# Kernel optimization log

Hardware: AMD Instinct MI355X
Metric: run time of the kernel (lower is better)

## Reference

```python
import jax, jax.numpy as jnp
import numpy as np

DIM = 64      # fixed by fuse=BasicConv2d(64,64)
HEADS = 8
B, H, W = 16, 128, 128
CPH = DIM // HEADS  # 8 channels per head


def conv2d(x, w, groups=1, pad=1):
    # x: [B,C,H,W], w: [O, C//groups, kh, kw]
    return jax.lax.conv_general_dilated(
        x, w, window_strides=(1, 1), padding=[(pad, pad), (pad, pad)],
        dimension_numbers=("NCHW", "OIHW", "NCHW"), feature_group_count=groups)


def setup_inputs() -> dict:
    key = jax.random.key(0)
    ks = jax.random.split(key, 8)
    y = jax.random.normal(ks[0], (B, DIM, H, W), jnp.float32)
    # conv3d kernels collapse to their middle depth slice (depth-1 input, zero pad)
    w_qkv = jax.random.normal(ks[1], (3 * DIM, DIM), jnp.float32) * 0.05        # 1x1x1 qkv
    w_dw = jax.random.normal(ks[2], (3 * DIM, 1, 3, 3), jnp.float32) * 0.1      # depthwise 3x3
    w_proj = jax.random.normal(ks[3], (DIM, DIM), jnp.float32) * 0.05           # 1x1x1 project_out
    w_fc = jax.random.normal(ks[4], (9, 3 * HEADS), jnp.float32) * 0.1          # fc: 24->9
    b_fc = jnp.zeros((9,), jnp.float32)
    w_dep = jax.random.normal(ks[5], (DIM, 9, 3, 3), jnp.float32) * 0.1         # grouped: 72->64, groups=8
    b_dep = jnp.zeros((DIM,), jnp.float32)
    temperature = jnp.ones((HEADS, 1, 1), jnp.float32)
    w_fuse = jax.random.normal(ks[6], (DIM, DIM, 3, 3), jnp.float32) * 0.05     # fuse conv, no bias
    bn_gamma = jnp.ones((DIM,), jnp.float32)
    bn_beta = jnp.zeros((DIM,), jnp.float32)
    bn_mean = jnp.zeros((DIM,), jnp.float32)
    bn_var = jnp.ones((DIM,), jnp.float32)
    return dict(y=y, w_qkv=w_qkv, w_dw=w_dw, w_proj=w_proj, w_fc=w_fc, b_fc=b_fc,
                w_dep=w_dep, b_dep=b_dep, temperature=temperature, w_fuse=w_fuse,
                bn_gamma=bn_gamma, bn_beta=bn_beta, bn_mean=bn_mean, bn_var=bn_var)


def reference(y, w_qkv, w_dw, w_proj, w_fc, b_fc, w_dep, b_dep, temperature,
              w_fuse, bn_gamma, bn_beta, bn_mean, bn_var):
    b, c, h, w = y.shape
    # qkv 1x1 conv then 3x3 depthwise conv (groups = 3*DIM)
    qkv = jnp.einsum('oc,bchw->bohw', w_qkv, y)                 # [b,192,h,w]
    qkv = conv2d(qkv, w_dw, groups=3 * DIM, pad=1)
    # dynamic kernel generation branch: flat reshape (row-major, matches torch)
    f_all = qkv.reshape(b, h * w, 3 * HEADS, CPH).transpose(0, 2, 1, 3)  # [b,24,hw,8]
    f_all = jnp.einsum('oc,bcne->bone', w_fc, f_all) + b_fc[None, :, None, None]  # [b,9,hw,8]
    f_conv = f_all.transpose(0, 3, 1, 2).reshape(b, 9 * CPH, h, w)       # [b,72,h,w]
    out_conv = conv2d(f_conv, w_dep, groups=CPH, pad=1) + b_dep[None, :, None, None]
    # channel (transposed) attention with L2-normalize + temperature + softmax
    q, k, v = jnp.split(qkv, 3, axis=1)
    def to_heads(t):
        return t.reshape(b, HEADS, CPH, h * w)
    q, k, v = to_heads(q), to_heads(k), to_heads(v)
    q = q / jnp.maximum(jnp.linalg.norm(q, axis=-1, keepdims=True), 1e-12)
    k = k / jnp.maximum(jnp.linalg.norm(k, axis=-1, keepdims=True), 1e-12)
    attn = jnp.einsum('bhcn,bhdn->bhcd', q, k) * temperature[None]       # [b,8,8,8]
    attn = jax.nn.softmax(attn, axis=-1)
    out = jnp.einsum('bhcd,bhdn->bhcn', attn, v).reshape(b, DIM, h, w)
    out = jnp.einsum('oc,bchw->bohw', w_proj, out)
    output = out + out_conv
    # fuse: conv3x3 (no bias) + BatchNorm (inference stats), then residual + ReLU
    fused = conv2d(output, w_fuse, pad=1)
    scale = (bn_gamma / jnp.sqrt(bn_var + 1e-5))[None, :, None, None]
    fused = (fused - bn_mean[None, :, None, None]) * scale + bn_beta[None, :, None, None]
    return jax.nn.relu(fused + y)
```

## Files before the change

kernel.cpp:

```cpp
#include <hip/hip_runtime.h>
#include <hip/hip_bf16.h>

#define BN 16
#define CC 64
#define HH 128
#define WW 128
#define HW 16384
#define C3 192
#define NHEADS 8


__global__ __launch_bounds__(256) void k_qkv1(const float* __restrict__ y,
                                              const float* __restrict__ w_qkv,
                                              float* __restrict__ out, int chunk) {
    __shared__ float ws[64 * 64];
    int tid = threadIdx.x;
    for (int i = tid; i < 4096; i += 256) {
        int c = i >> 6, o = i & 63;
        ws[i] = w_qkv[(chunk * 64 + o) * 64 + c];
    }
    __syncthreads();
    int bid = blockIdx.x;
    int b = bid >> 6;
    int ptile = bid & 63;
    int pxg = tid & 127;
    int osub = tid >> 7;
    int p0 = ptile * 256 + pxg * 2;
    const float* yb = y + (size_t)b * CC * HW + p0;
    float acc0[32];
    float acc1[32];
#pragma unroll
    for (int o = 0; o < 32; ++o) { acc0[o] = 0.f; acc1[o] = 0.f; }
    for (int c = 0; c < 64; ++c) {
        float2 yv = *(const float2*)(yb + (size_t)c * HW);
        const float* wr = &ws[c * 64 + osub * 32];
#pragma unroll
        for (int o = 0; o < 32; ++o) {
            float w = wr[o];
            acc0[o] = fmaf(w, yv.x, acc0[o]);
            acc1[o] = fmaf(w, yv.y, acc1[o]);
        }
    }
    float* ob = out + (size_t)b * 64 * HW + (size_t)(osub * 32) * HW + p0;
#pragma unroll
    for (int o = 0; o < 32; ++o) {
        *(float2*)(ob + (size_t)o * HW) = make_float2(acc0[o], acc1[o]);
    }
}

__global__ __launch_bounds__(256) void k_dw(const float* __restrict__ in,
                                            const float* __restrict__ w_dw,
                                            float* __restrict__ out, int chunk) {
    int bid = blockIdx.x;
    int tid = threadIdx.x;
    int b = bid >> 11;
    int rem = bid & 2047;
    int ch = rem >> 5;
    int tile = rem & 31;
    int pp = tile * 512 + tid * 2;
    int py = pp >> 7, px = pp & 127;
    const float* ib = in + ((size_t)b * 64 + ch) * HW;
    const float* wr = w_dw + (chunk * 64 + ch) * 9;
    float w[9];
#pragma unroll
    for (int i = 0; i < 9; ++i) w[i] = wr[i];
    float a0 = 0.f, a1 = 0.f;
#pragma unroll
    for (int ky = 0; ky < 3; ++ky) {
        int yy = py + ky - 1;
        bool yok = (unsigned)yy < 128u;
#pragma unroll
        for (int kx = 0; kx < 4; ++kx) {
            int xx = px + kx - 1;
            bool ok = yok && ((unsigned)xx < 128u);
            float v = ok ? ib[yy * 128 + xx] : 0.f;
            if (kx < 3) a0 = fmaf(w[ky * 3 + kx], v, a0);
            if (kx > 0) a1 = fmaf(w[ky * 3 + kx - 1], v, a1);
        }
    }
    *(float2*)(out + ((size_t)b * C3 + chunk * 64 + ch) * HW + pp) = make_float2(a0, a1);
}

__global__ __launch_bounds__(256) void k_fc(const float* __restrict__ qkv,
                                            const float* __restrict__ w_fc,
                                            const float* __restrict__ b_fc,
                                            float* __restrict__ fconv) {
    __shared__ float wf[216];
    __shared__ float bf[9];
    int tid = threadIdx.x;
    if (tid < 216) wf[tid] = w_fc[tid];
    if (tid < 9) bf[tid] = b_fc[tid];
    __syncthreads();
    int bid = blockIdx.x;
    int b = bid >> 9;
    int rem = bid & 511;
    int n = rem * 32 + (tid >> 3);
    int e = tid & 7;
    const float* x = qkv + (size_t)b * C3 * HW + (size_t)n * 192 + e;
    float xe[24];
#pragma unroll
    for (int g = 0; g < 24; ++g) xe[g] = x[g * 8];
    float* ob = fconv + (size_t)b * 72 * HW + n;
#pragma unroll
    for (int o = 0; o < 9; ++o) {
        float acc = bf[o];
#pragma unroll
        for (int g = 0; g < 24; ++g) acc = fmaf(wf[o * 24 + g], xe[g], acc);
        ob[(size_t)(e * 9 + o) * HW] = acc;
    }
}

#define GST 20
__global__ __launch_bounds__(256) void k_gconv(const float* __restrict__ fconv,
                                               const float* __restrict__ w_dep,
                                               const float* __restrict__ b_dep,
                                               float* __restrict__ outO) {
    __shared__ __align__(16) float sm_in[9 * 18 * GST];
    __shared__ __align__(16) float sm_w[81 * 8];
    __shared__ float sm_b[8];
    int tid = threadIdx.x;
    int bid = blockIdx.x;
    int b = bid >> 9;
    int rem = bid & 511;
    int grp = rem >> 6;
    int tile = rem & 63;
    int ty0 = (tile >> 3) * 16, tx0 = (tile & 7) * 16;
    const float* ibase = fconv + ((size_t)b * 72 + grp * 9) * HW;
    for (int i = tid; i < 9 * 324; i += 256) {
        int c = i / 324;
        int r2 = i - c * 324;
        int r = r2 / 18;
        int q = r2 - r * 18;
        int yy = ty0 + r - 1, xx = tx0 + q - 1;
        sm_in[c * (18 * GST) + r * GST + q] =
            ((unsigned)yy < 128u && (unsigned)xx < 128u)
                ? ibase[(size_t)c * HW + yy * 128 + xx] : 0.f;
    }
    for (int i = tid; i < 648; i += 256) {
        int o = i & 7;
        int ik = i >> 3;
        sm_w[i] = w_dep[(size_t)(grp * 8 + o) * 81 + ik];
    }
    if (tid < 8) sm_b[tid] = b_dep[grp * 8 + tid];
    __syncthreads();
    int row = tid >> 4, col = tid & 15;
    float acc[8];
#pragma unroll
    for (int o = 0; o < 8; ++o) acc[o] = sm_b[o];
#pragma unroll
    for (int ic = 0; ic < 9; ++ic) {
        float nb[3][3];
        const float* sc = &sm_in[ic * (18 * GST) + row * GST + col];
#pragma unroll
        for (int r = 0; r < 3; ++r)
#pragma unroll
            for (int q = 0; q < 3; ++q) nb[r][q] = sc[r * GST + q];
        const float* wp = &sm_w[ic * 72];
#pragma unroll
        for (int k = 0; k < 9; ++k) {
            float4 w0 = *(const float4*)(wp + k * 8);
            float4 w1 = *(const float4*)(wp + k * 8 + 4);
            float v = nb[k / 3][k % 3];
            acc[0] = fmaf(w0.x, v, acc[0]);
            acc[1] = fmaf(w0.y, v, acc[1]);
            acc[2] = fmaf(w0.z, v, acc[2]);
            acc[3] = fmaf(w0.w, v, acc[3]);
            acc[4] = fmaf(w1.x, v, acc[4]);
            acc[5] = fmaf(w1.y, v, acc[5]);
            acc[6] = fmaf(w1.z, v, acc[6]);
            acc[7] = fmaf(w1.w, v, acc[7]);
        }
    }
    float* ob = outO + ((size_t)b * 64 + grp * 8) * HW + (ty0 + row) * 128 + tx0 + col;
#pragma unroll
    for (int o = 0; o < 8; ++o) ob[(size_t)o * HW] = acc[o];
}

__global__ __launch_bounds__(256) void k_attn(const float* __restrict__ qkv,
                                              const float* __restrict__ temperature,
                                              float* __restrict__ attn) {
    __shared__ float red[4][64];
    __shared__ float redq[4][8];
    __shared__ float redk[4][8];
    __shared__ float sm_inv[16];
    __shared__ float lg[64];
    int bid = blockIdx.x;
    int b = bid >> 3, h = bid & 7;
    int tid = threadIdx.x;
    const float* Q = qkv + ((size_t)b * C3 + h * 8) * HW;
    const float* K = Q + (size_t)64 * HW;
    float acc[64], qs[8], ks[8];
#pragma unroll
    for (int j = 0; j < 64; ++j) acc[j] = 0.f;
#pragma unroll
    for (int d = 0; d < 8; ++d) { qs[d] = 0.f; ks[d] = 0.f; }
    for (int i = tid; i < HW; i += 256) {
        float qv[8], kv[8];
#pragma unroll
        for (int d = 0; d < 8; ++d) {
            qv[d] = Q[(size_t)d * HW + i];
            kv[d] = K[(size_t)d * HW + i];
        }
#pragma unroll
        for (int d = 0; d < 8; ++d) {
            qs[d] = fmaf(qv[d], qv[d], qs[d]);
            ks[d] = fmaf(kv[d], kv[d], ks[d]);
        }
#pragma unroll
        for (int c = 0; c < 8; ++c)
#pragma unroll
            for (int d = 0; d < 8; ++d)
                acc[c * 8 + d] = fmaf(qv[c], kv[d], acc[c * 8 + d]);
    }
#pragma unroll
    for (int j = 0; j < 64; ++j) {
#pragma unroll
        for (int off = 32; off; off >>= 1) acc[j] += __shfl_down(acc[j], off, 64);
    }
#pragma unroll
    for (int d = 0; d < 8; ++d) {
#pragma unroll
        for (int off = 32; off; off >>= 1) {
            qs[d] += __shfl_down(qs[d], off, 64);
            ks[d] += __shfl_down(ks[d], off, 64);
        }
    }
    int lane = tid & 63, wv = tid >> 6;
    if (lane == 0) {
#pragma unroll
        for (int j = 0; j < 64; ++j) red[wv][j] = acc[j];
#pragma unroll
        for (int d = 0; d < 8; ++d) { redq[wv][d] = qs[d]; redk[wv][d] = ks[d]; }
    }
    __syncthreads();
    if (tid < 16) {
        int d = tid & 7;
        float s = (tid < 8) ? (redq[0][d] + redq[1][d] + redq[2][d] + redq[3][d])
                            : (redk[0][d] + redk[1][d] + redk[2][d] + redk[3][d]);
        sm_inv[tid] = 1.f / fmaxf(sqrtf(s), 1e-12f);
    }
    __syncthreads();
    if (tid < 64) {
        float s = red[0][tid] + red[1][tid] + red[2][tid] + red[3][tid];
        int c = tid >> 3, d = tid & 7;
        lg[tid] = s * sm_inv[c] * sm_inv[8 + d] * temperature[h];
    }
    __syncthreads();
    if (tid < 8) {
        int c = tid;
        float m = lg[c * 8];
#pragma unroll
        for (int d = 1; d < 8; ++d) m = fmaxf(m, lg[c * 8 + d]);
        float ssum = 0.f, ex[8];
#pragma unroll
        for (int d = 0; d < 8; ++d) { ex[d] = expf(lg[c * 8 + d] - m); ssum += ex[d]; }
        float inv = 1.f / ssum;
#pragma unroll
        for (int d = 0; d < 8; ++d)
            attn[((size_t)(b * 8 + h) * 8 + c) * 8 + d] = ex[d] * inv;
    }
}

__global__ __launch_bounds__(256) void k_av_proj(const float* __restrict__ qkv,
                                                 const float* __restrict__ attn,
                                                 const float* __restrict__ w_proj,
                                                 float* __restrict__ outO) {
    __shared__ float at[512];
    __shared__ float wp[4096];
    int tid = threadIdx.x;
    int bid = blockIdx.x;
    int b = bid >> 6, tile = bid & 63;
    for (int i = tid; i < 512; i += 256) at[i] = attn[b * 512 + i];
    for (int i = tid; i < 4096; i += 256) {
        int c = i >> 6, o = i & 63;
        wp[i] = w_proj[o * 64 + c];
    }
    __syncthreads();
    int p = tile * 256 + tid;
    const float* vb = qkv + ((size_t)b * C3 + 128) * HW + p;
    float av[64];
#pragma unroll
    for (int h = 0; h < 8; ++h) {
        float vv[8];
#pragma unroll
        for (int d = 0; d < 8; ++d) vv[d] = vb[(size_t)(h * 8 + d) * HW];
#pragma unroll
        for (int ci = 0; ci < 8; ++ci) {
            float s = 0.f;
#pragma unroll
            for (int d = 0; d < 8; ++d) s = fmaf(at[(h * 8 + ci) * 8 + d], vv[d], s);
            av[h * 8 + ci] = s;
        }
    }
    float* ob = outO + (size_t)b * 64 * HW + p;
    float acc[64];
#pragma unroll
    for (int o = 0; o < 64; ++o) acc[o] = ob[(size_t)o * HW];
    for (int c = 0; c < 64; ++c) {
        float a = av[c];
        const float* wr = &wp[c * 64];
#pragma unroll
        for (int o = 0; o < 64; ++o) acc[o] = fmaf(wr[o], a, acc[o]);
    }
#pragma unroll
    for (int o = 0; o < 64; ++o) ob[(size_t)o * HW] = acc[o];
}

#define ST 20
__global__ __launch_bounds__(256) void k_fuse(const float* __restrict__ outO,
                                              const float* __restrict__ w_fuse,
                                              const float* __restrict__ bn_gamma,
                                              const float* __restrict__ bn_beta,
                                              const float* __restrict__ bn_mean,
                                              const float* __restrict__ bn_var,
                                              const float* __restrict__ y,
                                              float* __restrict__ dout) {
    __shared__ __align__(16) float sm_in[8 * 18 * ST];
    __shared__ __align__(16) float sm_w[8 * 9 * 64];
    __shared__ float sm_sc[64];
    __shared__ float sm_sb[64];
    int tid = threadIdx.x;
    int bid = blockIdx.x;
    int b = bid >> 6;
    int tile = bid & 63;
    int ty0 = (tile >> 3) * 16, tx0 = (tile & 7) * 16;

    if (tid < 64) {
        float sc = bn_gamma[tid] * rsqrtf(bn_var[tid] + 1e-5f);
        sm_sc[tid] = sc;
        sm_sb[tid] = bn_beta[tid] - bn_mean[tid] * sc;
    }

    int osub = tid >> 6;
    int o0 = osub * 16;
    int lane = tid & 63;
    int col = lane & 15;
    int rowg = lane >> 4;
    int r0 = rowg * 4;

    const float* ib = outO + (size_t)b * 64 * HW;
    float acc[4][16];
#pragma unroll
    for (int p = 0; p < 4; ++p)
#pragma unroll
        for (int o = 0; o < 16; ++o) acc[p][o] = 0.f;

    for (int ch = 0; ch < 8; ++ch) {
        int c0 = ch * 8;
        __syncthreads();
        for (int i = tid; i < 8 * 18 * 18; i += 256) {
            int c = i / 324;
            int rem = i - c * 324;
            int r = rem / 18;
            int q = rem - r * 18;
            int yy = ty0 + r - 1;
            int xx = tx0 + q - 1;
            float v = ((unsigned)yy < 128u && (unsigned)xx < 128u)
                          ? ib[(size_t)(c0 + c) * HW + yy * 128 + xx] : 0.f;
            sm_in[c * (18 * ST) + r * ST + q] = v;
        }
        for (int i = tid; i < 8 * 9 * 64; i += 256) {
            int o = i & 63;
            int kk = (i >> 6) % 9;
            int c = i / 576;
            sm_w[(c * 9 + kk) * 64 + o] = w_fuse[((size_t)o * 64 + (c0 + c)) * 9 + kk];
        }
        __syncthreads();
        for (int cc = 0; cc < 8; ++cc) {
            float nb[6][3];
            const float* sin_c = &sm_in[cc * (18 * ST)];
#pragma unroll
            for (int r = 0; r < 6; ++r)
#pragma unroll
                for (int q = 0; q < 3; ++q)
                    nb[r][q] = sin_c[(r0 + r) * ST + col + q];
            const float* wc = &sm_w[cc * 576 + o0];
#pragma unroll
            for (int k = 0; k < 9; ++k) {
                int ky = k / 3, kx = k % 3;
                float4 w0 = *(const float4*)(wc + k * 64);
                float4 w1 = *(const float4*)(wc + k * 64 + 4);
                float4 w2 = *(const float4*)(wc + k * 64 + 8);
                float4 w3 = *(const float4*)(wc + k * 64 + 12);
#pragma unroll
                for (int p = 0; p < 4; ++p) {
                    float v = nb[p + ky][kx];
                    acc[p][0]  = fmaf(w0.x, v, acc[p][0]);
                    acc[p][1]  = fmaf(w0.y, v, acc[p][1]);
                    acc[p][2]  = fmaf(w0.z, v, acc[p][2]);
                    acc[p][3]  = fmaf(w0.w, v, acc[p][3]);
                    acc[p][4]  = fmaf(w1.x, v, acc[p][4]);
                    acc[p][5]  = fmaf(w1.y, v, acc[p][5]);
                    acc[p][6]  = fmaf(w1.z, v, acc[p][6]);
                    acc[p][7]  = fmaf(w1.w, v, acc[p][7]);
                    acc[p][8]  = fmaf(w2.x, v, acc[p][8]);
                    acc[p][9]  = fmaf(w2.y, v, acc[p][9]);
                    acc[p][10] = fmaf(w2.z, v, acc[p][10]);
                    acc[p][11] = fmaf(w2.w, v, acc[p][11]);
                    acc[p][12] = fmaf(w3.x, v, acc[p][12]);
                    acc[p][13] = fmaf(w3.y, v, acc[p][13]);
                    acc[p][14] = fmaf(w3.z, v, acc[p][14]);
                    acc[p][15] = fmaf(w3.w, v, acc[p][15]);
                }
            }
        }
    }
#pragma unroll
    for (int o = 0; o < 16; ++o) {
        int og = o0 + o;
        float sc = sm_sc[og], sb = sm_sb[og];
#pragma unroll
        for (int p = 0; p < 4; ++p) {
            int pyy = ty0 + r0 + p;
            int pxx = tx0 + col;
            size_t idx = ((size_t)b * 64 + og) * HW + pyy * 128 + pxx;
            float v = acc[p][o] * sc + sb + y[idx];
            dout[idx] = fmaxf(v, 0.f);
        }
    }
}

extern "C" void kernel_launch(void* const* d_in, const int* in_sizes, int n_in,
                              void* d_out, int out_size, void* d_ws, size_t ws_size,
                              hipStream_t stream) {
    const float* y           = (const float*)d_in[0];
    const float* w_qkv       = (const float*)d_in[1];
    const float* w_dw        = (const float*)d_in[2];
    const float* w_proj      = (const float*)d_in[3];
    const float* w_fc        = (const float*)d_in[4];
    const float* b_fc        = (const float*)d_in[5];
    const float* w_dep       = (const float*)d_in[6];
    const float* b_dep       = (const float*)d_in[7];
    const float* temperature = (const float*)d_in[8];
    const float* w_fuse      = (const float*)d_in[9];
    const float* bn_gamma    = (const float*)d_in[10];
    const float* bn_beta     = (const float*)d_in[11];
    const float* bn_mean     = (const float*)d_in[12];
    const float* bn_var      = (const float*)d_in[13];
    float* out = (float*)d_out;

    float* ws    = (float*)d_ws;
    float* qkvB  = ws;
    float* bufT  = ws + 25165824;
    float* bufO  = ws + 34603008;
    float* attn  = ws + 42992640;
    (void)in_sizes; (void)n_in; (void)out_size; (void)ws_size;

    for (int g = 0; g < 2; ++g) {
        const float* yg = y + (size_t)g * 8 * CC * HW;
        float* outg = out + (size_t)g * 8 * CC * HW;
        for (int chunk = 0; chunk < 3; ++chunk) {
            k_qkv1<<<512, 256, 0, stream>>>(yg, w_qkv, bufT, chunk);
            k_dw<<<16384, 256, 0, stream>>>(bufT, w_dw, qkvB, chunk);
        }
        k_fc<<<4096, 256, 0, stream>>>(qkvB, w_fc, b_fc, bufT);
        k_gconv<<<4096, 256, 0, stream>>>(bufT, w_dep, b_dep, bufO);
        k_attn<<<64, 256, 0, stream>>>(qkvB, temperature, attn);
        k_av_proj<<<512, 256, 0, stream>>>(qkvB, attn, w_proj, bufO);
        k_fuse<<<512, 256, 0, stream>>>(bufO, w_fuse, bn_gamma, bn_beta,
                                        bn_mean, bn_var, yg, outg);
    }
}
```

Measured before the change: 1.045 ms.

## Fuse qkv 1x1 conv with depthwise 3x3 via haloed tiles; split fuse conv outputs

Replaces the separate qkv pointwise GEMM and depthwise conv launches with one kernel. Each block computes the 1x1 projection for a 16x16 tile plus its halo into shared memory, then applies the 3x3 depthwise filter there, so the intermediate never goes through global memory. The cost is recomputing the halo pixels (324 vs 256 per tile) and re-reading y once per group of 32 output channels. Separately, the fuse conv now splits its 64 output channels across two blocks, doubling the grid to raise occupancy and cut registers per thread, at the price of loading the input tile twice.

New measurement: 2.017 ms. +93.0%, slower.

```diff
diff --git a/kernel.cpp b/kernel.cpp
--- a/kernel.cpp
+++ b/kernel.cpp
@@ -10,75 +10,85 @@
 #define NHEADS 8
 
 
-__global__ __launch_bounds__(256) void k_qkv1(const float* __restrict__ y,
-                                              const float* __restrict__ w_qkv,
-                                              float* __restrict__ out, int chunk) {
-    __shared__ float ws[64 * 64];
-    int tid = threadIdx.x;
-    for (int i = tid; i < 4096; i += 256) {
-        int c = i >> 6, o = i & 63;
-        ws[i] = w_qkv[(chunk * 64 + o) * 64 + c];
-    }
-    __syncthreads();
-    int bid = blockIdx.x;
-    int b = bid >> 6;
-    int ptile = bid & 63;
-    int pxg = tid & 127;
-    int osub = tid >> 7;
-    int p0 = ptile * 256 + pxg * 2;
-    const float* yb = y + (size_t)b * CC * HW + p0;
-    float acc0[32];
-    float acc1[32];
+__global__ __launch_bounds__(256) void k_qkvdw(const float* __restrict__ y,
+                                               const float* __restrict__ w_qkv,
+                                               const float* __restrict__ w_dw,
+                                               float* __restrict__ qkvB) {
+    __shared__ __align__(16) float sm_w1[64 * 32];
+    __shared__ __align__(16) float sm_y[8 * 324];
+    __shared__ __align__(16) float sm_q[32 * 324];
+    __shared__ float sm_wd[32 * 9];
+    int tid = threadIdx.x;
+    int bid = blockIdx.x;
+    int b = bid / 384;
+    int rem = bid - b * 384;
+    int tile = rem / 6;
+    int q32 = rem - tile * 6;
+    int ty0 = (tile >> 3) * 16, tx0 = (tile & 7) * 16;
+
+    for (int i = tid; i < 2048; i += 256) {
+        int c = i >> 5, o = i & 31;
+        sm_w1[i] = w_qkv[(size_t)(q32 * 32 + o) * 64 + c];
+    }
+    for (int i = tid; i < 288; i += 256)
+        sm_wd[i] = w_dw[(size_t)(q32 * 32) * 9 + i];
+
+    const float* yb = y + (size_t)b * CC * HW;
+    float acc0[32], acc1[32];
 #pragma unroll
     for (int o = 0; o < 32; ++o) { acc0[o] = 0.f; acc1[o] = 0.f; }
-    for (int c = 0; c < 64; ++c) {
-        float2 yv = *(const float2*)(yb + (size_t)c * HW);
-        const float* wr = &ws[c * 64 + osub * 32];
-#pragma unroll
-        for (int o = 0; o < 32; ++o) {
-            float w = wr[o];
-            acc0[o] = fmaf(w, yv.x, acc0[o]);
-            acc1[o] = fmaf(w, yv.y, acc1[o]);
-        }
-    }
-    float* ob = out + (size_t)b * 64 * HW + (size_t)(osub * 32) * HW + p0;
+    bool p2 = tid < 68;
+
+    for (int c8 = 0; c8 < 8; ++c8) {
+        __syncthreads();
+        for (int i = tid; i < 2592; i += 256) {
+            int c = i / 324;
+            int p = i - c * 324;
+            int r = p / 18, q = p - r * 18;
+            int yy = ty0 + r - 1, xx = tx0 + q - 1;
+            sm_y[i] = ((unsigned)yy < 128u && (unsigned)xx < 128u)
+                          ? yb[(size_t)(c8 * 8 + c) * HW + yy * 128 + xx] : 0.f;
+        }
+        __syncthreads();
+#pragma unroll
+        for (int cc = 0; cc < 8; ++cc) {
+            float yv0 = sm_y[cc * 324 + tid];
+            float yv1 = p2 ? sm_y[cc * 324 + 256 + tid] : 0.f;
+            const float* wr = &sm_w1[(c8 * 8 + cc) * 32];
+#pragma unroll
+            for (int o4 = 0; o4 < 8; ++o4) {
+                float4 w = *(const float4*)(wr + o4 * 4);
+                acc0[o4 * 4 + 0] = fmaf(w.x, yv0, acc0[o4 * 4 + 0]);
+                acc0[o4 * 4 + 1] = fmaf(w.y, yv0, acc0[o4 * 4 + 1]);
+                acc0[o4 * 4 + 2] = fmaf(w.z, yv0, acc0[o4 * 4 + 2]);
+                acc0[o4 * 4 + 3] = fmaf(w.w, yv0, acc0[o4 * 4 + 3]);
+                acc1[o4 * 4 + 0] = fmaf(w.x, yv1, acc1[o4 * 4 + 0]);
+                acc1[o4 * 4 + 1] = fmaf(w.y, yv1, acc1[o4 * 4 + 1]);
+                acc1[o4 * 4 + 2] = fmaf(w.z, yv1, acc1[o4 * 4 + 2]);
+                acc1[o4 * 4 + 3] = fmaf(w.w, yv1, acc1[o4 * 4 + 3]);
+            }
+        }
+    }
 #pragma unroll
     for (int o = 0; o < 32; ++o) {
-        *(float2*)(ob + (size_t)o * HW) = make_float2(acc0[o], acc1[o]);
-    }
-}
-
-__global__ __launch_bounds__(256) void k_dw(const float* __restrict__ in,
-                                            const float* __restrict__ w_dw,
-                                            float* __restrict__ out, int chunk) {
-    int bid = blockIdx.x;
-    int tid = threadIdx.x;
-    int b = bid >> 11;
-    int rem = bid & 2047;
-    int ch = rem >> 5;
-    int tile = rem & 31;
-    int pp = tile * 512 + tid * 2;
-    int py = pp >> 7, px = pp & 127;
-    const float* ib = in + ((size_t)b * 64 + ch) * HW;
-    const float* wr = w_dw + (chunk * 64 + ch) * 9;
-    float w[9];
-#pragma unroll
-    for (int i = 0; i < 9; ++i) w[i] = wr[i];
-    float a0 = 0.f, a1 = 0.f;
-#pragma unroll
-    for (int ky = 0; ky < 3; ++ky) {
-        int yy = py + ky - 1;
-        bool yok = (unsigned)yy < 128u;
-#pragma unroll
-        for (int kx = 0; kx < 4; ++kx) {
-            int xx = px + kx - 1;
-            bool ok = yok && ((unsigned)xx < 128u);
-            float v = ok ? ib[yy * 128 + xx] : 0.f;
-            if (kx < 3) a0 = fmaf(w[ky * 3 + kx], v, a0);
-            if (kx > 0) a1 = fmaf(w[ky * 3 + kx - 1], v, a1);
-        }
-    }
-    *(float2*)(out + ((size_t)b * C3 + chunk * 64 + ch) * HW + pp) = make_float2(a0, a1);
+        sm_q[o * 324 + tid] = acc0[o];
+        if (p2) sm_q[o * 324 + 256 + tid] = acc1[o];
+    }
+    __syncthreads();
+    int row = tid >> 4, col = tid & 15;
+    float* ob = qkvB + ((size_t)b * C3 + q32 * 32) * HW
+                + (ty0 + row) * 128 + tx0 + col;
+    for (int ch = 0; ch < 32; ++ch) {
+        const float* sq = &sm_q[ch * 324 + row * 18 + col];
+        const float* wd = &sm_wd[ch * 9];
+        float a = 0.f;
+#pragma unroll
+        for (int dy = 0; dy < 3; ++dy)
+#pragma unroll
+            for (int dx = 0; dx < 3; ++dx)
+                a = fmaf(wd[dy * 3 + dx], sq[dy * 18 + dx], a);
+        ob[(size_t)ch * HW] = a;
+    }
 }
 
 __global__ __launch_bounds__(256) void k_fc(const float* __restrict__ qkv,
@@ -316,13 +326,15 @@
                                               const float* __restrict__ y,
                                               float* __restrict__ dout) {
     __shared__ __align__(16) float sm_in[8 * 18 * ST];
-    __shared__ __align__(16) float sm_w[8 * 9 * 64];
+    __shared__ __align__(16) float sm_w[8 * 9 * 32];
     __shared__ float sm_sc[64];
     __shared__ float sm_sb[64];
     int tid = threadIdx.x;
     int bid = blockIdx.x;
-    int b = bid >> 6;
-    int tile = bid & 63;
+    int b = bid >> 7;
+    int rem = bid & 127;
+    int ob32 = rem >> 6;
+    int tile = rem & 63;
     int ty0 = (tile >> 3) * 16, tx0 = (tile & 7) * 16;
 
     if (tid < 64) {
@@ -332,38 +344,39 @@
     }
 
     int osub = tid >> 6;
-    int o0 = osub * 16;
+    int o0 = osub * 8;
     int lane = tid & 63;
     int col = lane & 15;
     int rowg = lane >> 4;
     int r0 = rowg * 4;
 
     const float* ib = outO + (size_t)b * 64 * HW;
-    float acc[4][16];
+    float acc[4][8];
 #pragma unroll
     for (int p = 0; p < 4; ++p)
 #pragma unroll
-        for (int o = 0; o < 16; ++o) acc[p][o] = 0.f;
+        for (int o = 0; o < 8; ++o) acc[p][o] = 0.f;
 
     for (int ch = 0; ch < 8; ++ch) {
         int c0 = ch * 8;
         __syncthreads();
         for (int i = tid; i < 8 * 18 * 18; i += 256) {
             int c = i / 324;
-            int rem = i - c * 324;
-            int r = rem / 18;
-            int q = rem - r * 18;
+            int rem2 = i - c * 324;
+            int r = rem2 / 18;
+            int q = rem2 - r * 18;
             int yy = ty0 + r - 1;
             int xx = tx0 + q - 1;
             float v = ((unsigned)yy < 128u && (unsigned)xx < 128u)
                           ? ib[(size_t)(c0 + c) * HW + yy * 128 + xx] : 0.f;
             sm_in[c * (18 * ST) + r * ST + q] = v;
         }
-        for (int i = tid; i < 8 * 9 * 64; i += 256) {
-            int o = i & 63;
-            int kk = (i >> 6) % 9;
-            int c = i / 576;
-            sm_w[(c * 9 + kk) * 64 + o] = w_fuse[((size_t)o * 64 + (c0 + c)) * 9 + kk];
+        for (int i = tid; i < 8 * 9 * 32; i += 256) {
+            int o = i & 31;
+            int kk = (i >> 5) % 9;
+            int c = i / 288;
+            sm_w[(c * 9 + kk) * 32 + o] =
+                w_fuse[((size_t)(ob32 * 32 + o) * 64 + (c0 + c)) * 9 + kk];
         }
         __syncthreads();
         for (int cc = 0; cc < 8; ++cc) {
@@ -374,40 +387,30 @@
 #pragma unroll
                 for (int q = 0; q < 3; ++q)
                     nb[r][q] = sin_c[(r0 + r) * ST + col + q];
-            const float* wc = &sm_w[cc * 576 + o0];
+            const float* wc = &sm_w[cc * 288 + o0];
 #pragma unroll
             for (int k = 0; k < 9; ++k) {
                 int ky = k / 3, kx = k % 3;
-                float4 w0 = *(const float4*)(wc + k * 64);
-                float4 w1 = *(const float4*)(wc + k * 64 + 4);
-                float4 w2 = *(const float4*)(wc + k * 64 + 8);
-                float4 w3 = *(const float4*)(wc + k * 64 + 12);
+                float4 w0 = *(const float4*)(wc + k * 32);
+                float4 w1 = *(const float4*)(wc + k * 32 + 4);
 #pragma unroll
                 for (int p = 0; p < 4; ++p) {
                     float v = nb[p + ky][kx];
-                    acc[p][0]  = fmaf(w0.x, v, acc[p][0]);
-                    acc[p][1]  = fmaf(w0.y, v, acc[p][1]);
-                    acc[p][2]  = fmaf(w0.z, v, acc[p][2]);
-                    acc[p][3]  = fmaf(w0.w, v, acc[p][3]);
-                    acc[p][4]  = fmaf(w1.x, v, acc[p][4]);
-                    acc[p][5]  = fmaf(w1.y, v, acc[p][5]);
-                    acc[p][6]  = fmaf(w1.z, v, acc[p][6]);
-                    acc[p][7]  = fmaf(w1.w, v, acc[p][7]);
-                    acc[p][8]  = fmaf(w2.x, v, acc[p][8]);
-                    acc[p][9]  = fmaf(w2.y, v, acc[p][9]);
-                    acc[p][10] = fmaf(w2.z, v, acc[p][10]);
-                    acc[p][11] = fmaf(w2.w, v, acc[p][11]);
-                    acc[p][12] = fmaf(w3.x, v, acc[p][12]);
-                    acc[p][13] = fmaf(w3.y, v, acc[p][13]);
-                    acc[p][14] = fmaf(w3.z, v, acc[p][14]);
-                    acc[p][15] = fmaf(w3.w, v, acc[p][15]);
+                    acc[p][0] = fmaf(w0.x, v, acc[p][0]);
+                    acc[p][1] = fmaf(w0.y, v, acc[p][1]);
+                    acc[p][2] = fmaf(w0.z, v, acc[p][2]);
+                    acc[p][3] = fmaf(w0.w, v, acc[p][3]);
+                    acc[p][4] = fmaf(w1.x, v, acc[p][4]);
+                    acc[p][5] = fmaf(w1.y, v, acc[p][5]);
+                    acc[p][6] = fmaf(w1.z, v, acc[p][6]);
+                    acc[p][7] = fmaf(w1.w, v, acc[p][7]);
                 }
             }
         }
     }
 #pragma unroll
-    for (int o = 0; o < 16; ++o) {
-        int og = o0 + o;
+    for (int o = 0; o < 8; ++o) {
+        int og = ob32 * 32 + o0 + o;
         float sc = sm_sc[og], sb = sm_sb[og];
 #pragma unroll
         for (int p = 0; p < 4; ++p) {
@@ -449,15 +452,12 @@
     for (int g = 0; g < 2; ++g) {
         const float* yg = y + (size_t)g * 8 * CC * HW;
         float* outg = out + (size_t)g * 8 * CC * HW;
-        for (int chunk = 0; chunk < 3; ++chunk) {
-            k_qkv1<<<512, 256, 0, stream>>>(yg, w_qkv, bufT, chunk);
-            k_dw<<<16384, 256, 0, stream>>>(bufT, w_dw, qkvB, chunk);
-        }
+        k_qkvdw<<<3072, 256, 0, stream>>>(yg, w_qkv, w_dw, qkvB);
         k_fc<<<4096, 256, 0, stream>>>(qkvB, w_fc, b_fc, bufT);
         k_gconv<<<4096, 256, 0, stream>>>(bufT, w_dep, b_dep, bufO);
         k_attn<<<64, 256, 0, stream>>>(qkvB, temperature, attn);
         k_av_proj<<<512, 256, 0, stream>>>(qkvB, attn, w_proj, bufO);
-        k_fuse<<<512, 256, 0, stream>>>(bufO, w_fuse, bn_gamma, bn_beta,
-                                        bn_mean, bn_var, yg, outg);
-    }
-}
+        k_fuse<<<1024, 256, 0, stream>>>(bufO, w_fuse, bn_gamma, bn_beta,
+                                         bn_mean, bn_var, yg, outg);
+    }
+}
```
